# Kernel tuning notes

Hardware: AMD Instinct MI355X
Metric: run time of the kernel (lower is better)

Reference implementation:

```python
import jax, jax.numpy as jnp
import numpy as np

# Dimensions: B batch, I genes per case, E embed dim, V sga vocab, NH heads,
# NB attention blocks, CAN cancer types, OUT output genes
B, I, E, V, NH, NB, CAN, OUT = 128, 800, 512, 19000, 8, 4, 10, 5000
MASK_VAL = -1e9


def setup_inputs() -> dict:
    key = jax.random.key(0)
    ks = jax.random.split(key, 10)
    s = 0.02
    sga = jax.random.randint(ks[0], (B, I), 0, V)            # 0 == padding
    can = jax.random.randint(ks[1], (B,), 0, CAN)
    emb_tables = jax.random.normal(ks[2], (NB, V + 1, E), jnp.float32) * s
    emb_tables = emb_tables.at[:, 0, :].set(0.0)              # padding_idx=0
    Wk = jax.random.normal(ks[3], (NB, E, E), jnp.float32) * s   # transform2Keys
    bk = jnp.zeros((NB, E), jnp.float32)
    Wq = jax.random.normal(ks[4], (NB, E, NH), jnp.float32) * s  # queryKeyMatch
    bq = jnp.zeros((NB, NH), jnp.float32)
    can_emb = jax.random.normal(ks[5], (CAN, E), jnp.float32) * s
    Wh = jax.random.normal(ks[6], (NB - 1, E, E), jnp.float32) * s  # residual linears (no bias)
    Wfinal = jax.random.normal(ks[7], (E, OUT), jnp.float32) * s    # final linear (no bias)
    return dict(sga=sga, can=can, emb_tables=emb_tables, Wk=Wk, bk=bk,
                Wq=Wq, bq=bq, can_emb=can_emb, Wh=Wh, Wfinal=Wfinal)


def _sga_block(sga, table, Wk_b, bk_b, Wq_b, bq_b):
    embs = table[sga]                                   # [B,I,E] gather
    keys = jnp.tanh(embs @ Wk_b + bk_b)                 # [B,I,E]
    scores = keys @ Wq_b + bq_b                         # [B,I,NH]
    scores = jnp.where(sga[..., None] == 0, MASK_VAL, scores)
    A = jax.nn.softmax(scores, axis=1)                  # softmax over genes I
    emb = jnp.einsum('bin,bie->be', A, embs)            # sum over heads + genes
    attn_wt = A.sum(axis=2)                             # [B,I]
    return emb, attn_wt


def reference(sga, can, emb_tables, Wk, bk, Wq, bq, can_emb, Wh, Wfinal):
    emb0, attn0 = _sga_block(sga, emb_tables[0], Wk[0], bk[0], Wq[0], bq[0])
    curr = jax.nn.relu(emb0 + can_emb[can])             # using_cancer_type=True
    attns = [attn0]
    hiddens = [curr]
    for i in range(1, NB):
        emb_i, attn_i = _sga_block(sga, emb_tables[i], Wk[i], bk[i], Wq[i], bq[i])
        curr = emb_i + curr @ Wh[i - 1]
        curr = jax.nn.relu(curr) if i < NB - 1 else jax.nn.sigmoid(curr)
        attns.append(attn_i)
        hiddens.append(curr)
    preds = curr @ Wfinal                               # [B,OUT]
    return preds, jnp.stack(attns), jnp.stack(hiddens)
```

## Files before the change

kernel.cpp:

```cpp
#include <hip/hip_runtime.h>
#include <hip/hip_bf16.h>

constexpr int Bn   = 128;
constexpr int In   = 800;
constexpr int En   = 512;
constexpr int V1   = 19001;
constexpr int NHn  = 8;
constexpr int NBn  = 4;
constexpr int OUTn = 5000;

constexpr int OFF_ATTN = Bn * OUTn;
constexpr int OFF_HID  = OFF_ATTN + NBn * Bn * In;

typedef __attribute__((ext_vector_type(8))) short bf16x8;
typedef __attribute__((ext_vector_type(8))) unsigned short u16x8;
typedef __attribute__((ext_vector_type(4))) float f32x4;

__device__ inline ushort f2bf(float x) {
    __hip_bfloat16 h = __float2bfloat16(x);
    return *reinterpret_cast<ushort*>(&h);
}
__device__ inline float bf2f(ushort u) {
    return __uint_as_float(((unsigned)u) << 16);
}
__device__ inline void gl_lds16(const ushort* g, ushort* l) {
    __builtin_amdgcn_global_load_lds(
        (const __attribute__((address_space(1))) void*)g,
        (__attribute__((address_space(3))) void*)l, 16, 0, 0);
}

__global__ __launch_bounds__(256)
void k_prep(const float* __restrict__ Wk, ushort* __restrict__ Wkt) {
    __shared__ float ts[64][65];
    const int n0 = blockIdx.x * 64, k0 = blockIdx.y * 64, nb = blockIdx.z;
    const int t = threadIdx.x;
    {
        const int kr = t >> 2, nc = (t & 3) * 16;
        const float* p = Wk + (((size_t)nb * En) + (k0 + kr)) * En + n0 + nc;
#pragma unroll
        for (int j = 0; j < 4; ++j) {
            const float4 v = *(const float4*)(p + j * 4);
            ts[kr][nc + j * 4 + 0] = v.x; ts[kr][nc + j * 4 + 1] = v.y;
            ts[kr][nc + j * 4 + 2] = v.z; ts[kr][nc + j * 4 + 3] = v.w;
        }
    }
    __syncthreads();
    {
        const int nr = t >> 2, kc = (t & 3) * 16;
        ushort* d = Wkt + (((size_t)nb * En) + (n0 + nr)) * En + k0 + kc;
        ushort4 o;
#pragma unroll
        for (int j = 0; j < 4; ++j) {
            o.x = f2bf(ts[kc + j * 4 + 0][nr]); o.y = f2bf(ts[kc + j * 4 + 1][nr]);
            o.z = f2bf(ts[kc + j * 4 + 2][nr]); o.w = f2bf(ts[kc + j * 4 + 3][nr]);
            *(ushort4*)(d + j * 4) = o;
        }
    }
}

template <bool TBF>
__global__ __launch_bounds__(256, 2)
void k_scores(const float* __restrict__ T, const ushort* __restrict__ Wkt,
              const float* __restrict__ bk, const float* __restrict__ Wq,
              float* __restrict__ scoresv, ushort* __restrict__ Tbf) {
    __shared__ ushort Bs[2][512][32];
    __shared__ union { ushort A[2][64][32]; float red[4][64][NHn]; } u;

    const int mblk = blockIdx.x, nb = blockIdx.y;
    const int v0 = mblk * 64;
    const int tid = threadIdx.x, lane = tid & 63, w = tid >> 6;
    const int q = lane >> 4, c = lane & 15;

    const float*  Tb = T + (size_t)nb * V1 * En;
    const ushort* Wn = Wkt + (size_t)nb * En * En;

    const int arow = tid >> 2, akq = tid & 3;
    const int vra = v0 + arow;
    const float* agp = Tb + (size_t)vra * En + akq * 8;
    ushort* tsp = Tbf + ((size_t)nb * V1 + vra) * En + akq * 8;

    f32x4 acc[4][8];
#pragma unroll
    for (int mt = 0; mt < 4; ++mt)
#pragma unroll
        for (int nt = 0; nt < 8; ++nt) acc[mt][nt] = (f32x4)0.0f;

    auto stageB = [&](int buf, int k0) {
#pragma unroll
        for (int j = 0; j < 8; ++j) {
            const int nrow = (w * 8 + j) * 16;
            const ushort* gp =
                Wn + (size_t)(nrow + (lane >> 2)) * En + k0 + (lane & 3) * 8;
            gl_lds16(gp, &Bs[buf][nrow][0]);
        }
    };
    auto loadA = [&](int k0, float4& f0, float4& f1) {
        if (vra < V1) {
            f0 = *(const float4*)(agp + k0);
            f1 = *(const float4*)(agp + k0 + 4);
        } else {
            f0 = make_float4(0.f, 0.f, 0.f, 0.f);
            f1 = f0;
        }
    };
    auto writeA = [&](int buf, int k0, float4 f0, float4 f1) {
        u16x8 o;
        o[0] = f2bf(f0.x); o[1] = f2bf(f0.y); o[2] = f2bf(f0.z); o[3] = f2bf(f0.w);
        o[4] = f2bf(f1.x); o[5] = f2bf(f1.y); o[6] = f2bf(f1.z); o[7] = f2bf(f1.w);
        *(u16x8*)&u.A[buf][arow][akq * 8] = o;
        if (TBF && vra < V1) *(u16x8*)(tsp + k0) = o;
    };

    stageB(0, 0);
    {
        float4 f0, f1;
        loadA(0, f0, f1);
        writeA(0, 0, f0, f1);
    }
    __syncthreads();

    for (int it = 0; it < 16; ++it) {
        const int cur = it & 1, nxt = cur ^ 1;
        const int k0n = (it + 1) * 32;
        float4 p0, p1;
        if (it < 15) {
            stageB(nxt, k0n);
            loadA(k0n, p0, p1);
        }
        bf16x8 aF[4], bF[8];
#pragma unroll
        for (int mt = 0; mt < 4; ++mt)
            aF[mt] = *(bf16x8*)&u.A[cur][mt * 16 + c][q * 8];
#pragma unroll
        for (int nt = 0; nt < 8; ++nt)
            bF[nt] = *(bf16x8*)&Bs[cur][w * 128 + nt * 16 + c][q * 8];
#pragma unroll
        for (int nt = 0; nt < 8; ++nt)
#pragma unroll
            for (int mt = 0; mt < 4; ++mt)
                acc[mt][nt] = __builtin_amdgcn_mfma_f32_16x16x32_bf16(
                    aF[mt], bF[nt], acc[mt][nt], 0, 0, 0);
        if (it < 15) writeA(nxt, k0n, p0, p1);
        __syncthreads();
    }

#pragma unroll
    for (int nt = 0; nt < 8; ++nt) {
        const int col = w * 128 + nt * 16 + c;
        const float bkv = bk[nb * En + col];
#pragma unroll
        for (int mt = 0; mt < 4; ++mt)
#pragma unroll
            for (int r = 0; r < 4; ++r)
                acc[mt][nt][r] = tanhf(acc[mt][nt][r] + bkv);
    }

    for (int h = 0; h < NHn; ++h) {
        float wqh[8];
#pragma unroll
        for (int nt = 0; nt < 8; ++nt) {
            const int col = w * 128 + nt * 16 + c;
            wqh[nt] = Wq[((size_t)nb * En + col) * NHn + h];
        }
        float p[4][4];
#pragma unroll
        for (int mt = 0; mt < 4; ++mt)
#pragma unroll
            for (int r = 0; r < 4; ++r) {
                float s = 0.f;
#pragma unroll
                for (int nt = 0; nt < 8; ++nt) s += acc[mt][nt][r] * wqh[nt];
                p[mt][r] = s;
            }
#pragma unroll
        for (int m = 1; m < 16; m <<= 1) {
#pragma unroll
            for (int mt = 0; mt < 4; ++mt)
#pragma unroll
                for (int r = 0; r < 4; ++r)
                    p[mt][r] += __shfl_xor(p[mt][r], m, 64);
        }
        if (c == h) {
#pragma unroll
            for (int mt = 0; mt < 4; ++mt)
#pragma unroll
                for (int r = 0; r < 4; ++r)
                    u.red[w][mt * 16 + q * 4 + r][h] = p[mt][r];
        }
    }
    __syncthreads();

    for (int idx = tid; idx < 64 * NHn; idx += 256) {
        const int row = idx >> 3, h = idx & 7;
        const int vr = v0 + row;
        if (vr < V1)
            scoresv[((size_t)nb * V1 + vr) * NHn + h] =
                u.red[0][row][h] + u.red[1][row][h] +
                u.red[2][row][h] + u.red[3][row][h];
    }
}

__global__ __launch_bounds__(256)
void k_softmax(const int* __restrict__ sga, const float* __restrict__ scoresv,
               float* __restrict__ attn_out) {
    const int b  = blockIdx.x;
    const int nb = blockIdx.y;
    const int tid = threadIdx.x;
    const int lane = tid & 63;
    const int wid  = tid >> 6;
    __shared__ float red[4 * NHn];

    float sc[4][NHn];
    int ivals[4];
#pragma unroll
    for (int s = 0; s < 4; ++s) {
        const int i = tid + s * 256;
        ivals[s] = i;
        if (i < In) {
            const int v = sga[b * In + i];
            const float4 s0 = *(const float4*)(scoresv + ((size_t)nb * V1 + v) * NHn);
            const float4 s1 = *(const float4*)(scoresv + ((size_t)nb * V1 + v) * NHn + 4);
            sc[s][0] = s0.x; sc[s][1] = s0.y; sc[s][2] = s0.z; sc[s][3] = s0.w;
            sc[s][4] = s1.x; sc[s][5] = s1.y; sc[s][6] = s1.z; sc[s][7] = s1.w;
            if (v == 0) {
#pragma unroll
                for (int n = 0; n < NHn; ++n) sc[s][n] = -1e9f;
            }
        } else {
#pragma unroll
            for (int n = 0; n < NHn; ++n) sc[s][n] = -3.0e38f;
        }
    }

    float lm[NHn];
#pragma unroll
    for (int n = 0; n < NHn; ++n)
        lm[n] = fmaxf(fmaxf(sc[0][n], sc[1][n]), fmaxf(sc[2][n], sc[3][n]));
#pragma unroll
    for (int m = 1; m < 64; m <<= 1) {
#pragma unroll
        for (int n = 0; n < NHn; ++n) lm[n] = fmaxf(lm[n], __shfl_xor(lm[n], m, 64));
    }
    if (lane == 0) {
#pragma unroll
        for (int n = 0; n < NHn; ++n) red[wid * NHn + n] = lm[n];
    }
    __syncthreads();
    float M[NHn];
#pragma unroll
    for (int n = 0; n < NHn; ++n)
        M[n] = fmaxf(fmaxf(red[n], red[NHn + n]), fmaxf(red[2 * NHn + n], red[3 * NHn + n]));
    __syncthreads();

    float ls[NHn];
#pragma unroll
    for (int n = 0; n < NHn; ++n) ls[n] = 0.f;
#pragma unroll
    for (int s = 0; s < 4; ++s) {
#pragma unroll
        for (int n = 0; n < NHn; ++n) {
            sc[s][n] = expf(sc[s][n] - M[n]);
            ls[n] += sc[s][n];
        }
    }
#pragma unroll
    for (int m = 1; m < 64; m <<= 1) {
#pragma unroll
        for (int n = 0; n < NHn; ++n) ls[n] += __shfl_xor(ls[n], m, 64);
    }
    if (lane == 0) {
#pragma unroll
        for (int n = 0; n < NHn; ++n) red[wid * NHn + n] = ls[n];
    }
    __syncthreads();
    float inv[NHn];
#pragma unroll
    for (int n = 0; n < NHn; ++n) {
        const float S = red[n] + red[NHn + n] + red[2 * NHn + n] + red[3 * NHn + n];
        inv[n] = 1.0f / S;
    }

#pragma unroll
    for (int s = 0; s < 4; ++s) {
        if (ivals[s] < In) {
            float w = 0.f;
#pragma unroll
            for (int n = 0; n < NHn; ++n) w += sc[s][n] * inv[n];
            attn_out[((size_t)nb * Bn + b) * In + ivals[s]] = w;
        }
    }
}

template <bool TBF>
__global__ __launch_bounds__(512)
void k_emb(const int* __restrict__ sga, const float* __restrict__ attn,
           const float* __restrict__ T, const ushort* __restrict__ Tbf,
           float* __restrict__ emb) {
    const int b  = blockIdx.x;
    const int nb = blockIdx.y;
    __shared__ int   sv[In];
    __shared__ float sw[In];
    __shared__ float pa[8][En];
    for (int idx = threadIdx.x; idx < In; idx += 512) {
        sv[idx] = sga[b * In + idx];
        sw[idx] = attn[((size_t)nb * Bn + b) * In + idx];
    }
    __syncthreads();
    const int wave = threadIdx.x >> 6, lane = threadIdx.x & 63;
    float a[8];
#pragma unroll
    for (int j = 0; j < 8; ++j) a[j] = 0.f;

    if (TBF) {
        const ushort* Tb = Tbf + (size_t)nb * V1 * En;
#pragma unroll 4
        for (int g = 0; g < 100; ++g) {
            const int i = wave * 100 + g;
            const int v = sv[i];
            const float w = sw[i];
            const u16x8 t = *(const u16x8*)(Tb + (size_t)v * En + lane * 8);
#pragma unroll
            for (int j = 0; j < 8; ++j) a[j] += w * bf2f(t[j]);
        }
    } else {
        const float* Tb = T + (size_t)nb * V1 * En;
#pragma unroll 4
        for (int g = 0; g < 100; ++g) {
            const int i = wave * 100 + g;
            const int v = sv[i];
            const float w = sw[i];
            const float4* p = (const float4*)(Tb + (size_t)v * En) + lane * 2;
            const float4 t0 = p[0], t1 = p[1];
            a[0] += w * t0.x; a[1] += w * t0.y; a[2] += w * t0.z; a[3] += w * t0.w;
            a[4] += w * t1.x; a[5] += w * t1.y; a[6] += w * t1.z; a[7] += w * t1.w;
        }
    }
#pragma unroll
    for (int j = 0; j < 8; ++j) pa[wave][lane * 8 + j] = a[j];
    __syncthreads();
    const int t = threadIdx.x;
    float s = 0.f;
#pragma unroll
    for (int wv = 0; wv < 8; ++wv) s += pa[wv][t];
    emb[((size_t)nb * Bn + b) * En + t] = s;
}

__global__ __launch_bounds__(256)
void k_step0(const float* __restrict__ emb0, const int* __restrict__ can,
             const float* __restrict__ can_emb, float* __restrict__ cur,
             float* __restrict__ hid) {
    const int b = blockIdx.x;
    const int e0 = threadIdx.x * 2;
    const int c = can[b];
    float2 v = *(const float2*)(emb0 + (size_t)b * En + e0);
    const float2 ce = *(const float2*)(can_emb + (size_t)c * En + e0);
    v.x = fmaxf(v.x + ce.x, 0.f);
    v.y = fmaxf(v.y + ce.y, 0.f);
    *(float2*)(cur + (size_t)b * En + e0) = v;
    *(float2*)(hid + (size_t)b * En + e0) = v;
}

__global__ __launch_bounds__(256)
void k_step(const float* __restrict__ embi, const float* __restrict__ prev,
            const float* __restrict__ Whi, float* __restrict__ cur,
            float* __restrict__ hid, const int sig) {
    const int b = blockIdx.x, cc = blockIdx.y;
    __shared__ float pr[En];
    __shared__ float part[2][128];
    pr[threadIdx.x]       = prev[(size_t)b * En + threadIdx.x];
    pr[threadIdx.x + 256] = prev[(size_t)b * En + threadIdx.x + 256];
    __syncthreads();
    const int col = cc * 128 + (threadIdx.x & 127);
    const int kh  = threadIdx.x >> 7;
    float s = 0.f;
    const float* Wp = Whi + (size_t)(kh * 256) * En + col;
#pragma unroll 8
    for (int k = 0; k < 256; ++k) s += pr[kh * 256 + k] * Wp[(size_t)k * En];
    part[kh][threadIdx.x & 127] = s;
    __syncthreads();
    if (threadIdx.x < 128) {
        float a = part[0][threadIdx.x] + part[1][threadIdx.x] +
                  embi[(size_t)b * En + col];
        if (sig) a = 1.0f / (1.0f + expf(-a));
        else     a = fmaxf(a, 0.f);
        cur[(size_t)b * En + col] = a;
        hid[(size_t)b * En + col] = a;
    }
}

__global__ __launch_bounds__(256, 2)
void k_preds(const float* __restrict__ cur, const float* __restrict__ Wf,
             float* __restrict__ preds) {
    __shared__ float cs[32 * En];
    const int nt = blockIdx.x;
    const int bt = blockIdx.y;
    for (int idx = threadIdx.x; idx < 32 * 128; idx += 256) {
        const int row = idx >> 7;
        const int c4  = (idx & 127) << 2;
        *(float4*)(cs + row * En + c4) =
            *(const float4*)(cur + (size_t)(bt * 32 + row) * En + c4);
    }
    __syncthreads();
    const int lane = threadIdx.x & 63;
    const int rgrp = threadIdx.x >> 6;
    const int col = nt * 64 + lane;
    float acc[8];
#pragma unroll
    for (int j = 0; j < 8; ++j) acc[j] = 0.f;
    const bool ok = (col < OUTn);
    for (int k = 0; k < En; k += 4) {
        float w0 = 0.f, w1 = 0.f, w2 = 0.f, w3 = 0.f;
        if (ok) {
            w0 = Wf[(size_t)(k + 0) * OUTn + col];
            w1 = Wf[(size_t)(k + 1) * OUTn + col];
            w2 = Wf[(size_t)(k + 2) * OUTn + col];
            w3 = Wf[(size_t)(k + 3) * OUTn + col];
        }
#pragma unroll
        for (int j = 0; j < 8; ++j) {
            const float4 cv = *(const float4*)(cs + (rgrp * 8 + j) * En + k);
            acc[j] += cv.x * w0 + cv.y * w1 + cv.z * w2 + cv.w * w3;
        }
    }
    if (ok) {
#pragma unroll
        for (int j = 0; j < 8; ++j)
            preds[(size_t)(bt * 32 + rgrp * 8 + j) * OUTn + col] = acc[j];
    }
}

extern "C" void kernel_launch(void* const* d_in, const int* in_sizes, int n_in,
                              void* d_out, int out_size, void* d_ws, size_t ws_size,
                              hipStream_t stream) {
    const int*   sga     = (const int*)d_in[0];
    const int*   can     = (const int*)d_in[1];
    const float* T       = (const float*)d_in[2];
    const float* Wk      = (const float*)d_in[3];
    const float* bk      = (const float*)d_in[4];
    const float* Wq      = (const float*)d_in[5];
    const float* can_emb = (const float*)d_in[7];
    const float* Wh      = (const float*)d_in[8];
    const float* Wf      = (const float*)d_in[9];

    float* out = (float*)d_out;
    float* ws  = (float*)d_ws;

    float* scoresv = ws;
    float* embw    = scoresv + (size_t)NBn * V1 * NHn;
    float* cur0    = embw + (size_t)NBn * Bn * En;
    float* cur1    = cur0 + (size_t)Bn * En;
    ushort* Wkt    = (ushort*)(cur1 + (size_t)Bn * En);
    ushort* Tbf    = Wkt + (size_t)NBn * En * En;
    const size_t need_full =
        (size_t)(scoresv - ws) * 4 +
        ((size_t)NBn * V1 * NHn + (size_t)NBn * Bn * En + 2 * (size_t)Bn * En) * 4 +
        (size_t)NBn * En * En * 2 + (size_t)NBn * V1 * En * 2;
    const bool useTbf = (ws_size >= need_full);

    float* preds_out = out;
    float* attn_out  = out + OFF_ATTN;
    float* hid_out   = out + OFF_HID;

    k_prep<<<dim3(8, 8, NBn), 256, 0, stream>>>(Wk, Wkt);
    if (useTbf)
        k_scores<true><<<dim3((V1 + 63) / 64, NBn), 256, 0, stream>>>(
            T, Wkt, bk, Wq, scoresv, Tbf);
    else
        k_scores<false><<<dim3((V1 + 63) / 64, NBn), 256, 0, stream>>>(
            T, Wkt, bk, Wq, scoresv, Tbf);
    k_softmax<<<dim3(Bn, NBn), 256, 0, stream>>>(sga, scoresv, attn_out);
    if (useTbf)
        k_emb<true><<<dim3(Bn, NBn), 512, 0, stream>>>(sga, attn_out, T, Tbf, embw);
    else
        k_emb<false><<<dim3(Bn, NBn), 512, 0, stream>>>(sga, attn_out, T, Tbf, embw);
    k_step0<<<Bn, 256, 0, stream>>>(embw, can, can_emb, cur0, hid_out);
    k_step<<<dim3(Bn, 4), 256, 0, stream>>>(embw + 1 * Bn * En, cur0,
                                            Wh + 0 * En * En, cur1,
                                            hid_out + 1 * (size_t)Bn * En, 0);
    k_step<<<dim3(Bn, 4), 256, 0, stream>>>(embw + 2 * Bn * En, cur1,
                                            Wh + 1 * En * En, cur0,
                                            hid_out + 2 * (size_t)Bn * En, 0);
    k_step<<<dim3(Bn, 4), 256, 0, stream>>>(embw + 3 * Bn * En, cur0,
                                            Wh + 2 * En * En, cur1,
                                            hid_out + 3 * (size_t)Bn * En, 1);
    k_preds<<<dim3((OUTn + 63) / 64, Bn / 32), 256, 0, stream>>>(cur1, Wf, preds_out);
}
```

Measured before the change: 577.0 us.

## Widen score kernel to 512 threads, use fast tanh and DPP reductions

```diff
diff --git a/kernel.cpp b/kernel.cpp
--- a/kernel.cpp
+++ b/kernel.cpp
@@ -28,6 +28,16 @@
         (const __attribute__((address_space(1))) void*)g,
         (__attribute__((address_space(3))) void*)l, 16, 0, 0);
 }
+
+__device__ inline float fast_tanh(float x) {
+    const float e = __expf(2.0f * x);
+    return 1.0f - 2.0f / (e + 1.0f);
+}
+
+#define DPP_XOR1(x) __int_as_float(__builtin_amdgcn_update_dpp( \
+    0, __float_as_int(x), 0xB1, 0xF, 0xF, false))
+#define DPP_XOR2(x) __int_as_float(__builtin_amdgcn_update_dpp( \
+    0, __float_as_int(x), 0x4E, 0xF, 0xF, false))
 
 __global__ __launch_bounds__(256)
 void k_prep(const float* __restrict__ Wk, ushort* __restrict__ Wkt) {
@@ -59,12 +69,12 @@
 }
 
 template <bool TBF>
-__global__ __launch_bounds__(256, 2)
+__global__ __launch_bounds__(512, 4)
 void k_scores(const float* __restrict__ T, const ushort* __restrict__ Wkt,
               const float* __restrict__ bk, const float* __restrict__ Wq,
               float* __restrict__ scoresv, ushort* __restrict__ Tbf) {
     __shared__ ushort Bs[2][512][32];
-    __shared__ union { ushort A[2][64][32]; float red[4][64][NHn]; } u;
+    __shared__ union { ushort A[2][64][32]; float red[8][64][NHn]; } u;
 
     const int mblk = blockIdx.x, nb = blockIdx.y;
     const int v0 = mblk * 64;
@@ -74,92 +84,86 @@
     const float*  Tb = T + (size_t)nb * V1 * En;
     const ushort* Wn = Wkt + (size_t)nb * En * En;
 
-    const int arow = tid >> 2, akq = tid & 3;
+    const int arow = tid >> 3, akq = tid & 7;
     const int vra = v0 + arow;
-    const float* agp = Tb + (size_t)vra * En + akq * 8;
-    ushort* tsp = Tbf + ((size_t)nb * V1 + vra) * En + akq * 8;
-
-    f32x4 acc[4][8];
+    const float* agp = Tb + (size_t)vra * En + akq * 4;
+    ushort* tsp = Tbf + ((size_t)nb * V1 + vra) * En + akq * 4;
+
+    f32x4 acc[4][4];
 #pragma unroll
     for (int mt = 0; mt < 4; ++mt)
 #pragma unroll
-        for (int nt = 0; nt < 8; ++nt) acc[mt][nt] = (f32x4)0.0f;
+        for (int nt = 0; nt < 4; ++nt) acc[mt][nt] = (f32x4)0.0f;
 
     auto stageB = [&](int buf, int k0) {
 #pragma unroll
-        for (int j = 0; j < 8; ++j) {
-            const int nrow = (w * 8 + j) * 16;
+        for (int j = 0; j < 4; ++j) {
+            const int nrow = (w * 4 + j) * 16;
             const ushort* gp =
                 Wn + (size_t)(nrow + (lane >> 2)) * En + k0 + (lane & 3) * 8;
             gl_lds16(gp, &Bs[buf][nrow][0]);
         }
     };
-    auto loadA = [&](int k0, float4& f0, float4& f1) {
-        if (vra < V1) {
-            f0 = *(const float4*)(agp + k0);
-            f1 = *(const float4*)(agp + k0 + 4);
-        } else {
-            f0 = make_float4(0.f, 0.f, 0.f, 0.f);
-            f1 = f0;
-        }
+    auto loadA = [&](int k0, float4& f0) {
+        if (vra < V1) f0 = *(const float4*)(agp + k0);
+        else          f0 = make_float4(0.f, 0.f, 0.f, 0.f);
     };
-    auto writeA = [&](int buf, int k0, float4 f0, float4 f1) {
-        u16x8 o;
-        o[0] = f2bf(f0.x); o[1] = f2bf(f0.y); o[2] = f2bf(f0.z); o[3] = f2bf(f0.w);
-        o[4] = f2bf(f1.x); o[5] = f2bf(f1.y); o[6] = f2bf(f1.z); o[7] = f2bf(f1.w);
-        *(u16x8*)&u.A[buf][arow][akq * 8] = o;
-        if (TBF && vra < V1) *(u16x8*)(tsp + k0) = o;
+    auto writeA = [&](int buf, int k0, float4 f0) {
+        ushort4 o;
+        o.x = f2bf(f0.x); o.y = f2bf(f0.y); o.z = f2bf(f0.z); o.w = f2bf(f0.w);
+        *(ushort4*)&u.A[buf][arow][akq * 4] = o;
+        if (TBF && vra < V1) *(ushort4*)(tsp + k0) = o;
     };
 
     stageB(0, 0);
     {
-        float4 f0, f1;
-        loadA(0, f0, f1);
-        writeA(0, 0, f0, f1);
+        float4 f0;
+        loadA(0, f0);
+        writeA(0, 0, f0);
     }
     __syncthreads();
 
     for (int it = 0; it < 16; ++it) {
         const int cur = it & 1, nxt = cur ^ 1;
         const int k0n = (it + 1) * 32;
-        float4 p0, p1;
+        float4 p0;
         if (it < 15) {
             stageB(nxt, k0n);
-            loadA(k0n, p0, p1);
-        }
-        bf16x8 aF[4], bF[8];
+            loadA(k0n, p0);
+        }
+        bf16x8 aF[4], bF[4];
 #pragma unroll
         for (int mt = 0; mt < 4; ++mt)
             aF[mt] = *(bf16x8*)&u.A[cur][mt * 16 + c][q * 8];
 #pragma unroll
-        for (int nt = 0; nt < 8; ++nt)
-            bF[nt] = *(bf16x8*)&Bs[cur][w * 128 + nt * 16 + c][q * 8];
-#pragma unroll
-        for (int nt = 0; nt < 8; ++nt)
+        for (int nt = 0; nt < 4; ++nt)
+            bF[nt] = *(bf16x8*)&Bs[cur][w * 64 + nt * 16 + c][q * 8];
+#pragma unroll
+        for (int nt = 0; nt < 4; ++nt)
 #pragma unroll
             for (int mt = 0; mt < 4; ++mt)
                 acc[mt][nt] = __builtin_amdgcn_mfma_f32_16x16x32_bf16(
                     aF[mt], bF[nt], acc[mt][nt], 0, 0, 0);
-        if (it < 15) writeA(nxt, k0n, p0, p1);
+        if (it < 15) writeA(nxt, k0n, p0);
         __syncthreads();
     }
 
 #pragma unroll
-    for (int nt = 0; nt < 8; ++nt) {
-        const int col = w * 128 + nt * 16 + c;
+    for (int nt = 0; nt < 4; ++nt) {
+        const int col = w * 64 + nt * 16 + c;
         const float bkv = bk[nb * En + col];
 #pragma unroll
         for (int mt = 0; mt < 4; ++mt)
 #pragma unroll
             for (int r = 0; r < 4; ++r)
-                acc[mt][nt][r] = tanhf(acc[mt][nt][r] + bkv);
+                acc[mt][nt][r] = fast_tanh(acc[mt][nt][r] + bkv);
     }
 
     for (int h = 0; h < NHn; ++h) {
-        float wqh[8];
-#pragma unroll
-        for (int nt = 0; nt < 8; ++nt) {
-            const int col = w * 128 + nt * 16 + c;
+        float wqh[4];
+#pragma unroll
+        for (int nt = 0; nt < 4; ++nt) {
+            const int col = w * 64 + nt * 16 + c;
             wqh[nt] = Wq[((size_t)nb * En + col) * NHn + h];
         }
         float p[4][4];
@@ -169,17 +173,13 @@
             for (int r = 0; r < 4; ++r) {
                 float s = 0.f;
 #pragma unroll
-                for (int nt = 0; nt < 8; ++nt) s += acc[mt][nt][r] * wqh[nt];
+                for (int nt = 0; nt < 4; ++nt) s += acc[mt][nt][r] * wqh[nt];
+                s += DPP_XOR1(s);
+                s += DPP_XOR2(s);
+                s += __shfl_xor(s, 4, 64);
+                s += __shfl_xor(s, 8, 64);
                 p[mt][r] = s;
             }
-#pragma unroll
-        for (int m = 1; m < 16; m <<= 1) {
-#pragma unroll
-            for (int mt = 0; mt < 4; ++mt)
-#pragma unroll
-                for (int r = 0; r < 4; ++r)
-                    p[mt][r] += __shfl_xor(p[mt][r], m, 64);
-        }
         if (c == h) {
 #pragma unroll
             for (int mt = 0; mt < 4; ++mt)
@@ -190,13 +190,15 @@
     }
     __syncthreads();
 
-    for (int idx = tid; idx < 64 * NHn; idx += 256) {
-        const int row = idx >> 3, h = idx & 7;
+    {
+        const int row = tid >> 3, h = tid & 7;
         const int vr = v0 + row;
-        if (vr < V1)
-            scoresv[((size_t)nb * V1 + vr) * NHn + h] =
-                u.red[0][row][h] + u.red[1][row][h] +
-                u.red[2][row][h] + u.red[3][row][h];
+        if (vr < V1) {
+            float s = 0.f;
+#pragma unroll
+            for (int wv = 0; wv < 8; ++wv) s += u.red[wv][row][h];
+            scoresv[((size_t)nb * V1 + vr) * NHn + h] = s;
+        }
     }
 }
 
@@ -313,7 +315,7 @@
 
     if (TBF) {
         const ushort* Tb = Tbf + (size_t)nb * V1 * En;
-#pragma unroll 4
+#pragma unroll 10
         for (int g = 0; g < 100; ++g) {
             const int i = wave * 100 + g;
             const int v = sv[i];
@@ -324,7 +326,7 @@
         }
     } else {
         const float* Tb = T + (size_t)nb * V1 * En;
-#pragma unroll 4
+#pragma unroll 10
         for (int g = 0; g < 100; ++g) {
             const int i = wave * 100 + g;
             const int v = sv[i];
@@ -463,10 +465,10 @@
 
     k_prep<<<dim3(8, 8, NBn), 256, 0, stream>>>(Wk, Wkt);
     if (useTbf)
-        k_scores<true><<<dim3((V1 + 63) / 64, NBn), 256, 0, stream>>>(
+        k_scores<true><<<dim3((V1 + 63) / 64, NBn), 512, 0, stream>>>(
             T, Wkt, bk, Wq, scoresv, Tbf);
     else
-        k_scores<false><<<dim3((V1 + 63) / 64, NBn), 256, 0, stream>>>(
+        k_scores<false><<<dim3((V1 + 63) / 64, NBn), 512, 0, stream>>>(
             T, Wkt, bk, Wq, scoresv, Tbf);
     k_softmax<<<dim3(Bn, NBn), 256, 0, stream>>>(sga, scoresv, attn_out);
     if (useTbf)
```

Result: slower. 627.4 us (+8.7%).

## Swizzle LDS tiles, use fast tanh and DPP reductions, batch bf16 stores

Applied to the files above, without the earlier changes.

```diff
diff --git a/kernel.cpp b/kernel.cpp
--- a/kernel.cpp
+++ b/kernel.cpp
@@ -28,6 +28,16 @@
         (const __attribute__((address_space(1))) void*)g,
         (__attribute__((address_space(3))) void*)l, 16, 0, 0);
 }
+
+__device__ inline float fast_tanh(float x) {
+    const float e = __expf(2.0f * x);
+    return 1.0f - 2.0f / (e + 1.0f);
+}
+
+#define DPP_XOR1(x) __int_as_float(__builtin_amdgcn_update_dpp( \
+    0, __float_as_int(x), 0xB1, 0xF, 0xF, false))
+#define DPP_XOR2(x) __int_as_float(__builtin_amdgcn_update_dpp( \
+    0, __float_as_int(x), 0x4E, 0xF, 0xF, false))
 
 __global__ __launch_bounds__(256)
 void k_prep(const float* __restrict__ Wk, ushort* __restrict__ Wkt) {
@@ -70,11 +80,13 @@
     const int v0 = mblk * 64;
     const int tid = threadIdx.x, lane = tid & 63, w = tid >> 6;
     const int q = lane >> 4, c = lane & 15;
+    const int gsw = (q ^ (c & 3)) * 8;
 
     const float*  Tb = T + (size_t)nb * V1 * En;
     const ushort* Wn = Wkt + (size_t)nb * En * En;
 
     const int arow = tid >> 2, akq = tid & 3;
+    const int aswz = (akq ^ (arow & 3)) * 8;
     const int vra = v0 + arow;
     const float* agp = Tb + (size_t)vra * En + akq * 8;
     ushort* tsp = Tbf + ((size_t)nb * V1 + vra) * En + akq * 8;
@@ -89,8 +101,9 @@
 #pragma unroll
         for (int j = 0; j < 8; ++j) {
             const int nrow = (w * 8 + j) * 16;
-            const ushort* gp =
-                Wn + (size_t)(nrow + (lane >> 2)) * En + k0 + (lane & 3) * 8;
+            const int r = nrow + (lane >> 2);
+            const int gf = (lane & 3) ^ ((lane >> 2) & 3);
+            const ushort* gp = Wn + (size_t)r * En + k0 + gf * 8;
             gl_lds16(gp, &Bs[buf][nrow][0]);
         }
     };
@@ -103,12 +116,21 @@
             f1 = f0;
         }
     };
+    u16x8 stash;
     auto writeA = [&](int buf, int k0, float4 f0, float4 f1) {
         u16x8 o;
         o[0] = f2bf(f0.x); o[1] = f2bf(f0.y); o[2] = f2bf(f0.z); o[3] = f2bf(f0.w);
         o[4] = f2bf(f1.x); o[5] = f2bf(f1.y); o[6] = f2bf(f1.z); o[7] = f2bf(f1.w);
-        *(u16x8*)&u.A[buf][arow][akq * 8] = o;
-        if (TBF && vra < V1) *(u16x8*)(tsp + k0) = o;
+        *(u16x8*)&u.A[buf][arow][aswz] = o;
+        if (TBF && vra < V1) {
+            const int itIdx = k0 >> 5;
+            if ((itIdx & 1) == 0) {
+                stash = o;
+            } else {
+                *(u16x8*)(tsp + k0 - 32) = stash;
+                *(u16x8*)(tsp + k0)      = o;
+            }
+        }
     };
 
     stageB(0, 0);
@@ -130,10 +152,10 @@
         bf16x8 aF[4], bF[8];
 #pragma unroll
         for (int mt = 0; mt < 4; ++mt)
-            aF[mt] = *(bf16x8*)&u.A[cur][mt * 16 + c][q * 8];
+            aF[mt] = *(bf16x8*)&u.A[cur][mt * 16 + c][gsw];
 #pragma unroll
         for (int nt = 0; nt < 8; ++nt)
-            bF[nt] = *(bf16x8*)&Bs[cur][w * 128 + nt * 16 + c][q * 8];
+            bF[nt] = *(bf16x8*)&Bs[cur][w * 128 + nt * 16 + c][gsw];
 #pragma unroll
         for (int nt = 0; nt < 8; ++nt)
 #pragma unroll
@@ -152,7 +174,7 @@
         for (int mt = 0; mt < 4; ++mt)
 #pragma unroll
             for (int r = 0; r < 4; ++r)
-                acc[mt][nt][r] = tanhf(acc[mt][nt][r] + bkv);
+                acc[mt][nt][r] = fast_tanh(acc[mt][nt][r] + bkv);
     }
 
     for (int h = 0; h < NHn; ++h) {
@@ -170,16 +192,12 @@
                 float s = 0.f;
 #pragma unroll
                 for (int nt = 0; nt < 8; ++nt) s += acc[mt][nt][r] * wqh[nt];
+                s += DPP_XOR1(s);
+                s += DPP_XOR2(s);
+                s += __shfl_xor(s, 4, 64);
+                s += __shfl_xor(s, 8, 64);
                 p[mt][r] = s;
             }
-#pragma unroll
-        for (int m = 1; m < 16; m <<= 1) {
-#pragma unroll
-            for (int mt = 0; mt < 4; ++mt)
-#pragma unroll
-                for (int r = 0; r < 4; ++r)
-                    p[mt][r] += __shfl_xor(p[mt][r], m, 64);
-        }
         if (c == h) {
 #pragma unroll
             for (int mt = 0; mt < 4; ++mt)
@@ -313,7 +331,7 @@
 
     if (TBF) {
         const ushort* Tb = Tbf + (size_t)nb * V1 * En;
-#pragma unroll 4
+#pragma unroll 10
         for (int g = 0; g < 100; ++g) {
             const int i = wave * 100 + g;
             const int v = sv[i];
@@ -324,7 +342,7 @@
         }
     } else {
         const float* Tb = T + (size_t)nb * V1 * En;
-#pragma unroll 4
+#pragma unroll 10
         for (int g = 0; g < 100; ++g) {
             const int i = wave * 100 + g;
             const int v = sv[i];
```

After: 544.9 us. 5.6% less time.
